# Performance work log

Hardware: AMD Instinct MI355X
Metric: run time of the kernel (lower is better)

The kernel has to match this reference:

```python
import jax, jax.numpy as jnp
import numpy as np

B, T, E, H = 4, 2048, 1024, 16
DH = E // H  # head_size = 64


def setup_inputs() -> dict:
    key = jax.random.key(0)
    ks = jax.random.split(key, 6)
    s_in = 1.0 / np.sqrt(E)
    return {
        "x": jax.random.normal(ks[0], (B, T, E), dtype=jnp.float32),
        "Wq": jax.random.normal(ks[1], (H, E, DH), dtype=jnp.float32) * s_in,
        "Wk": jax.random.normal(ks[2], (H, E, DH), dtype=jnp.float32) * s_in,
        "Wv": jax.random.normal(ks[3], (H, E, DH), dtype=jnp.float32) * s_in,
        "Wp": jax.random.normal(ks[4], (E, E), dtype=jnp.float32) * s_in,
        "bp": jax.random.normal(ks[5], (E,), dtype=jnp.float32) * 0.01,
    }


def reference(x, Wq, Wk, Wv, Wp, bp):
    # per-head q/k/v projections, batched over heads: [B,H,T,DH]
    q = jnp.einsum("bte,hed->bhtd", x, Wq)
    k = jnp.einsum("bte,hed->bhtd", x, Wk)
    v = jnp.einsum("bte,hed->bhtd", x, Wv)
    scale = 1.0 / jnp.sqrt(jnp.asarray(DH, dtype=x.dtype))
    scores = jnp.einsum("bhsd,bhtd->bhst", q, k) * scale  # [B,H,T,T]
    causal = jnp.tril(jnp.ones((T, T), dtype=bool))
    scores = jnp.where(causal, scores, jnp.asarray(-jnp.inf, dtype=scores.dtype))
    att = jax.nn.softmax(scores, axis=-1)
    out = jnp.einsum("bhst,bhtd->bhsd", att, v)  # [B,H,T,DH]
    # concat heads along last dim -> [B,T,E]
    out = out.transpose(0, 2, 1, 3).reshape(B, T, E)
    # output projection (dropout p=0.0 is identity)
    return out @ Wp.T + bp
```

## Files before the change

### kernel.cpp

```cpp
#include <hip/hip_runtime.h>
#include <hip/hip_bf16.h>

#define B_ 4
#define T_ 2048
#define E_ 1024
#define H_ 16
#define DH_ 64

typedef __bf16 bf16x8 __attribute__((ext_vector_type(8)));
typedef __bf16 bf16x4 __attribute__((ext_vector_type(4)));
typedef float f32x4 __attribute__((ext_vector_type(4)));

#define EXP2F(x) __builtin_amdgcn_exp2f(x)
#define NEG_INF (-__builtin_inff())

__device__ __forceinline__ void async_copy16(const __bf16* g, __bf16* l) {
    __builtin_amdgcn_global_load_lds(
        (const __attribute__((address_space(1))) unsigned int*)g,
        (__attribute__((address_space(3))) unsigned int*)l, 16, 0, 0);
}

__global__ void cast_f32_to_bf16(const float* __restrict__ src,
                                 __bf16* __restrict__ dst, int n) {
    int i = (blockIdx.x * blockDim.x + threadIdx.x) * 4;
    if (i + 3 < n) {
        float4 f = *reinterpret_cast<const float4*>(src + i);
        bf16x4 o = { (__bf16)f.x, (__bf16)f.y, (__bf16)f.z, (__bf16)f.w };
        *reinterpret_cast<bf16x4*>(dst + i) = o;
    }
}

__global__ void cast_wcat(const float* __restrict__ Wq, const float* __restrict__ Wk,
                          const float* __restrict__ Wv, __bf16* __restrict__ out) {
    int idx = blockIdx.x * blockDim.x + threadIdx.x;
    int e = idx & (E_ - 1);
    int n = idx >> 10;
    int rem = n & 1023, h = rem >> 6, d = rem & 63;
    const float* src = (n < 1024) ? Wq : (n < 2048 ? Wk : Wv);
    out[idx] = (__bf16)src[((h << 10) + e) * DH_ + d];
}

template<int MODE>
__global__ __launch_bounds__(256, 3) void gemm128(
    const __bf16* __restrict__ A, const __bf16* __restrict__ Bt,
    float* __restrict__ Cf, const float* __restrict__ bias,
    __bf16* __restrict__ oq, __bf16* __restrict__ ok, __bf16* __restrict__ ovt,
    int K, int N) {

    __shared__ __bf16 As[128][64];
    __shared__ __bf16 Bs[128][64];

    int tid = threadIdx.x, lane = tid & 63, wid = tid >> 6;
    int wr = wid >> 1, wc = wid & 1;
    int rlo = lane & 15, rhi = lane >> 4;
    int l8 = lane >> 3, c = lane & 7;

    const __bf16* Ab = A + (long)blockIdx.x * 128 * K;
    const __bf16* Bb = Bt + (long)blockIdx.y * 128 * K;

    f32x4 acc[4][4] = {};

    for (int k0 = 0; k0 < K; k0 += 64) {
        #pragma unroll
        for (int p = 0; p < 4; p++) {
            int gr = p * 32 + wid * 8 + l8;
            int sc = c ^ (gr & 7);
            async_copy16(Ab + (long)gr * K + k0 + sc * 8, &As[p * 32 + wid * 8][0]);
        }
        #pragma unroll
        for (int p = 0; p < 4; p++) {
            int gr = p * 32 + wid * 8 + l8;
            int sc = c ^ (gr & 7);
            async_copy16(Bb + (long)gr * K + k0 + sc * 8, &Bs[p * 32 + wid * 8][0]);
        }
        __syncthreads();

        #pragma unroll
        for (int kk = 0; kk < 2; kk++) {
            bf16x8 af[4], bfr[4];
            #pragma unroll
            for (int mi = 0; mi < 4; mi++) {
                int r = wr * 64 + mi * 16 + rlo;
                af[mi] = *reinterpret_cast<const bf16x8*>(
                    &As[r][((kk * 4 + rhi) ^ (r & 7)) * 8]);
            }
            #pragma unroll
            for (int ni = 0; ni < 4; ni++) {
                int r = wc * 64 + ni * 16 + rlo;
                bfr[ni] = *reinterpret_cast<const bf16x8*>(
                    &Bs[r][((kk * 4 + rhi) ^ (r & 7)) * 8]);
            }
            #pragma unroll
            for (int mi = 0; mi < 4; mi++)
                #pragma unroll
                for (int ni = 0; ni < 4; ni++)
                    acc[mi][ni] = __builtin_amdgcn_mfma_f32_16x16x32_bf16(
                        af[mi], bfr[ni], acc[mi][ni], 0, 0, 0);
        }
        __syncthreads();
    }

    long m0 = (long)blockIdx.x * 128 + wr * 64;
    int n0 = blockIdx.y * 128 + wc * 64;

    if constexpr (MODE == 1) {
        #pragma unroll
        for (int mi = 0; mi < 4; mi++) {
            #pragma unroll
            for (int ni = 0; ni < 4; ni++) {
                int cn = n0 + ni * 16 + rlo;
                #pragma unroll
                for (int r = 0; r < 4; r++) {
                    long rm = m0 + mi * 16 + rhi * 4 + r;
                    Cf[rm * N + cn] = acc[mi][ni][r] + bias[cn];
                }
            }
        }
    } else {
        int type = blockIdx.y >> 3;
        #pragma unroll
        for (int mi = 0; mi < 4; mi++) {
            long m_ = m0 + mi * 16 + rhi * 4;
            int b = (int)(m_ >> 11);
            int t0 = (int)(m_ & 2047);
            #pragma unroll
            for (int ni = 0; ni < 4; ni++) {
                int n = n0 + ni * 16 + rlo;
                int rem = n & 1023, h = rem >> 6, d = rem & 63;
                long bh = b * 16 + h;
                if (type == 2) {
                    bf16x4 o = { (__bf16)acc[mi][ni][0], (__bf16)acc[mi][ni][1],
                                 (__bf16)acc[mi][ni][2], (__bf16)acc[mi][ni][3] };
                    *reinterpret_cast<bf16x4*>(ovt + (bh * 64 + d) * 2048 + t0) = o;
                } else {
                    __bf16* dst = (type ? ok : oq) + bh * 2048 * 64;
                    #pragma unroll
                    for (int r = 0; r < 4; r++)
                        dst[(long)(t0 + r) * 64 + d] = (__bf16)acc[mi][ni][r];
                }
            }
        }
    }
}

__global__ __launch_bounds__(256, 4) void attn_kernel(
    const __bf16* __restrict__ q, const __bf16* __restrict__ k,
    const __bf16* __restrict__ vt, __bf16* __restrict__ attout) {

    __shared__ __bf16 Ks[2][64][64];
    __shared__ __bf16 Vs[2][64][64];
    __shared__ __bf16 Pl[4][16][64];

    int tid = threadIdx.x, lane = tid & 63, wid = tid >> 6;
    int rlo = lane & 15, rhi = lane >> 4;

    int fid = blockIdx.y * 16 + blockIdx.x;
    int xcd = fid & 7, slot = fid >> 3;
    int bh = xcd * 8 + (slot >> 4);
    int p = slot & 15;
    int tA = 31 - p, tB = p;

    int b = bh >> 4, h = bh & 15;
    const __bf16* qb = q + (long)bh * T_ * DH_;
    const __bf16* kb = k + (long)bh * T_ * DH_;
    const __bf16* vtb = vt + (long)bh * T_ * DH_;

    const float SCL = 0.125f * 1.44269504088896340736f;

    int srow = wid * 16 + (lane >> 3);
    int sc0 = (lane & 7) ^ (srow & 7);

    bf16x8 aqA[2], aqB[2];
    {
        long qrA = (long)tA * 64 + wid * 16 + rlo;
        aqA[0] = *reinterpret_cast<const bf16x8*>(qb + qrA * DH_ + 8 * rhi);
        aqA[1] = *reinterpret_cast<const bf16x8*>(qb + qrA * DH_ + 32 + 8 * rhi);
        long qrB = (long)tB * 64 + wid * 16 + rlo;
        aqB[0] = *reinterpret_cast<const bf16x8*>(qb + qrB * DH_ + 8 * rhi);
        aqB[1] = *reinterpret_cast<const bf16x8*>(qb + qrB * DH_ + 32 + 8 * rhi);
    }

    float mA = NEG_INF, lAc = 0.f, mB = NEG_INF, lBc = 0.f;
    f32x4 oA[4] = {}, oB[4] = {};

    auto STAGE = [&](int bs, int t) {
        const __bf16* ksrc = kb + (long)(t * 64 + srow) * DH_ + sc0 * 8;
        async_copy16(ksrc,           &Ks[bs][wid * 16][0]);
        async_copy16(ksrc + 8 * DH_, &Ks[bs][wid * 16 + 8][0]);
        const __bf16* vsrc = vtb + (long)srow * T_ + t * 64 + sc0 * 8;
        async_copy16(vsrc,           &Vs[bs][wid * 16][0]);
        async_copy16(vsrc + 8 * T_,  &Vs[bs][wid * 16 + 8][0]);
    };

    auto APPLYMASK = [&](f32x4* s, int qrow, int kt0) {
        int kbase = kt0 + rhi * 4;
        #pragma unroll
        for (int f = 0; f < 4; f++)
            #pragma unroll
            for (int r = 0; r < 4; r++)
                if (kbase + f * 16 + r > qrow) s[f][r] = NEG_INF;
    };

    auto SOFTMAX_PV = [&](int bs, f32x4* s, float& m_, float& l_, f32x4* o) {
        float pm;
        {
            f32x4 mx;
            #pragma unroll
            for (int r = 0; r < 4; r++)
                mx[r] = fmaxf(fmaxf(s[0][r], s[1][r]), fmaxf(s[2][r], s[3][r]));
            pm = fmaxf(fmaxf(mx[0], mx[1]), fmaxf(mx[2], mx[3]));
            pm = fmaxf(pm, __shfl_xor(pm, 16));
            pm = fmaxf(pm, __shfl_xor(pm, 32));
        }
        float pms = pm * SCL;

        bool need = !__all(pms <= m_ + 8.f);
        if (need) {
            float nm = fmaxf(m_, pms);
            float so = EXP2F(m_ - nm);
            m_ = nm;
            l_ *= so;
            float sov[4];
            #pragma unroll
            for (int r = 0; r < 4; r++) sov[r] = __shfl(so, rhi * 4 + r);
            #pragma unroll
            for (int fd = 0; fd < 4; fd++)
                #pragma unroll
                for (int r = 0; r < 4; r++)
                    o[fd][r] *= sov[r];
        }

        float rsum = 0.f;
        #pragma unroll
        for (int f = 0; f < 4; f++)
            #pragma unroll
            for (int r = 0; r < 4; r++) {
                float pv = EXP2F(fmaf(s[f][r], SCL, -m_));
                s[f][r] = pv;
                rsum += pv;
            }
        rsum += __shfl_xor(rsum, 16);
        rsum += __shfl_xor(rsum, 32);
        l_ += rsum;

        #pragma unroll
        for (int f = 0; f < 4; f++) {
            bf16x4 pw = { (__bf16)s[f][0], (__bf16)s[f][1],
                          (__bf16)s[f][2], (__bf16)s[f][3] };
            int keyb = f * 16 + rhi * 4;
            int c16 = keyb >> 3, sub = (keyb >> 2) & 1;
            *reinterpret_cast<bf16x4*>(
                &Pl[wid][rlo][((c16 ^ (rlo & 7)) << 3) + (sub << 2)]) = pw;
        }

        __builtin_amdgcn_s_setprio(1);
        #pragma unroll
        for (int kk = 0; kk < 2; kk++) {
            int ck = kk * 4 + rhi;
            bf16x8 ap = *reinterpret_cast<const bf16x8*>(&Pl[wid][rlo][(ck ^ (rlo & 7)) * 8]);
            #pragma unroll
            for (int fd = 0; fd < 4; fd++) {
                int vr = fd * 16 + rlo;
                bf16x8 bv = *reinterpret_cast<const bf16x8*>(
                    &Vs[bs][vr][(ck ^ (vr & 7)) * 8]);
                o[fd] = __builtin_amdgcn_mfma_f32_16x16x32_bf16(ap, bv, o[fd], 0, 0, 0);
            }
        }
        __builtin_amdgcn_s_setprio(0);
    };

    int qrowA = tA * 64 + wid * 16 + rlo;
    int qrowB = tB * 64 + wid * 16 + rlo;

    int nsteps = tA + 1;

    STAGE(0, 0);
    STAGE(1, 1);
    asm volatile("s_waitcnt vmcnt(4)" ::: "memory");
    asm volatile("s_barrier" ::: "memory");

    for (int t = 0; t < nsteps; ++t) {
        int cur = t & 1;
        bool doB = (t <= tB);

        f32x4 sA[4], sB[4];
        __builtin_amdgcn_s_setprio(1);
        #pragma unroll
        for (int f = 0; f < 4; f++) {
            int kr = f * 16 + rlo;
            bf16x8 ak0 = *reinterpret_cast<const bf16x8*>(
                &Ks[cur][kr][((0 + rhi) ^ (kr & 7)) * 8]);
            bf16x8 ak1 = *reinterpret_cast<const bf16x8*>(
                &Ks[cur][kr][((4 + rhi) ^ (kr & 7)) * 8]);
            f32x4 a0 = {};
            a0 = __builtin_amdgcn_mfma_f32_16x16x32_bf16(ak0, aqA[0], a0, 0, 0, 0);
            a0 = __builtin_amdgcn_mfma_f32_16x16x32_bf16(ak1, aqA[1], a0, 0, 0, 0);
            sA[f] = a0;
            if (doB) {
                f32x4 b0 = {};
                b0 = __builtin_amdgcn_mfma_f32_16x16x32_bf16(ak0, aqB[0], b0, 0, 0, 0);
                b0 = __builtin_amdgcn_mfma_f32_16x16x32_bf16(ak1, aqB[1], b0, 0, 0, 0);
                sB[f] = b0;
            }
        }
        __builtin_amdgcn_s_setprio(0);

        if (t == tA) APPLYMASK(sA, qrowA, t * 64);
        SOFTMAX_PV(cur, sA, mA, lAc, oA);
        if (doB) {
            if (t == tB) APPLYMASK(sB, qrowB, t * 64);
            SOFTMAX_PV(cur, sB, mB, lBc, oB);
        }

        asm volatile("s_barrier" ::: "memory");
        if (t + 2 < nsteps) {
            STAGE(cur, t + 2);
            asm volatile("s_waitcnt vmcnt(4)" ::: "memory");
        } else {
            asm volatile("s_waitcnt vmcnt(0)" ::: "memory");
        }
        asm volatile("s_barrier" ::: "memory");
    }

    float lvA[4], lvB[4];
    #pragma unroll
    for (int r = 0; r < 4; r++) {
        lvA[r] = __shfl(lAc, rhi * 4 + r);
        lvB[r] = __shfl(lBc, rhi * 4 + r);
    }
    #pragma unroll
    for (int r = 0; r < 4; r++) {
        float invA = 1.f / lvA[r];
        float invB = 1.f / lvB[r];
        long qrA = (long)tA * 64 + wid * 16 + rhi * 4 + r;
        long qrB = (long)tB * 64 + wid * 16 + rhi * 4 + r;
        #pragma unroll
        for (int fd = 0; fd < 4; fd++) {
            int d = fd * 16 + rlo;
            attout[((long)b * T_ + qrA) * E_ + h * DH_ + d] = (__bf16)(oA[fd][r] * invA);
            attout[((long)b * T_ + qrB) * E_ + h * DH_ + d] = (__bf16)(oB[fd][r] * invB);
        }
    }
}

extern "C" void kernel_launch(void* const* d_in, const int* in_sizes, int n_in,
                              void* d_out, int out_size, void* d_ws, size_t ws_size,
                              hipStream_t stream) {
    const float* x  = (const float*)d_in[0];
    const float* Wq = (const float*)d_in[1];
    const float* Wk = (const float*)d_in[2];
    const float* Wv = (const float*)d_in[3];
    const float* Wp = (const float*)d_in[4];
    const float* bp = (const float*)d_in[5];

    char* ws = (char*)d_ws;
    const long SZ_XE = (long)B_ * T_ * E_ * 2;
    __bf16* xb   = (__bf16*)(ws);
    __bf16* qb   = (__bf16*)(ws + SZ_XE);
    __bf16* kb   = (__bf16*)(ws + 2 * SZ_XE);
    __bf16* vt   = (__bf16*)(ws + 3 * SZ_XE);
    __bf16* wcat = (__bf16*)(ws + 4 * SZ_XE);
    __bf16* wpb  = (__bf16*)(ws + 4 * SZ_XE + (long)3072 * 1024 * 2);
    __bf16* att  = xb;

    cast_f32_to_bf16<<<8192, 256, 0, stream>>>(x, xb, B_ * T_ * E_);
    cast_wcat<<<12288, 256, 0, stream>>>(Wq, Wk, Wv, wcat);
    cast_f32_to_bf16<<<1024, 256, 0, stream>>>(Wp, wpb, E_ * E_);

    gemm128<3><<<dim3(64, 24), 256, 0, stream>>>(
        xb, wcat, nullptr, nullptr, qb, kb, vt, E_, 3 * E_);

    attn_kernel<<<dim3(16, B_ * H_), 256, 0, stream>>>(qb, kb, vt, att);

    gemm128<1><<<dim3(64, 8), 256, 0, stream>>>(
        att, wpb, (float*)d_out, bp, nullptr, nullptr, nullptr, E_, E_);
}
```

Measured before the change: 164.7 us.

## Fuse three cast kernels into one and defer softmax cross-lane reductions

Merges the x, Wq/Wk/Wv, and Wp casts into a single kernel launch, with the weight transpose-cast now handling 4 elements per thread. In the attention softmax, the row-max shuffle reduction runs only when a rescale is needed, and the row-sum shuffles move out of the loop to a single reduction at the end. This removes two launches and per-tile shuffle work, at the cost of strided scalar loads in the weight cast and per-lane max thresholds that rely on the lazy-rescale tolerance.

```diff
diff --git a/kernel.cpp b/kernel.cpp
--- a/kernel.cpp
+++ b/kernel.cpp
@@ -20,24 +20,34 @@
         (__attribute__((address_space(3))) unsigned int*)l, 16, 0, 0);
 }
 
-__global__ void cast_f32_to_bf16(const float* __restrict__ src,
-                                 __bf16* __restrict__ dst, int n) {
-    int i = (blockIdx.x * blockDim.x + threadIdx.x) * 4;
-    if (i + 3 < n) {
-        float4 f = *reinterpret_cast<const float4*>(src + i);
+__global__ void cast_all(const float* __restrict__ x,
+                         const float* __restrict__ Wq, const float* __restrict__ Wk,
+                         const float* __restrict__ Wv, const float* __restrict__ Wp,
+                         __bf16* __restrict__ xb, __bf16* __restrict__ wcat,
+                         __bf16* __restrict__ wpb) {
+    int tid = blockIdx.x * blockDim.x + threadIdx.x;
+    {
+        int i = tid * 4;
+        float4 f = *reinterpret_cast<const float4*>(x + i);
         bf16x4 o = { (__bf16)f.x, (__bf16)f.y, (__bf16)f.z, (__bf16)f.w };
-        *reinterpret_cast<bf16x4*>(dst + i) = o;
-    }
-}
-
-__global__ void cast_wcat(const float* __restrict__ Wq, const float* __restrict__ Wk,
-                          const float* __restrict__ Wv, __bf16* __restrict__ out) {
-    int idx = blockIdx.x * blockDim.x + threadIdx.x;
-    int e = idx & (E_ - 1);
-    int n = idx >> 10;
-    int rem = n & 1023, h = rem >> 6, d = rem & 63;
-    const float* src = (n < 1024) ? Wq : (n < 2048 ? Wk : Wv);
-    out[idx] = (__bf16)src[((h << 10) + e) * DH_ + d];
+        *reinterpret_cast<bf16x4*>(xb + i) = o;
+    }
+    if (tid < 262144) {
+        int i = tid * 4;
+        float4 f = *reinterpret_cast<const float4*>(Wp + i);
+        bf16x4 o = { (__bf16)f.x, (__bf16)f.y, (__bf16)f.z, (__bf16)f.w };
+        *reinterpret_cast<bf16x4*>(wpb + i) = o;
+    }
+    if (tid < 786432) {
+        int i = tid * 4;
+        int e = i & (E_ - 1);
+        int n = i >> 10;
+        int rem = n & 1023, h = rem >> 6, d = rem & 63;
+        const float* src = (n < 1024) ? Wq : (n < 2048 ? Wk : Wv);
+        const float* sp = src + ((long)((h << 10) + e)) * DH_ + d;
+        bf16x4 o = { (__bf16)sp[0], (__bf16)sp[DH_], (__bf16)sp[2 * DH_], (__bf16)sp[3 * DH_] };
+        *reinterpret_cast<bf16x4*>(wcat + i) = o;
+    }
 }
 
 template<int MODE>
@@ -202,21 +212,18 @@
     };
 
     auto SOFTMAX_PV = [&](int bs, f32x4* s, float& m_, float& l_, f32x4* o) {
-        float pm;
-        {
-            f32x4 mx;
-            #pragma unroll
-            for (int r = 0; r < 4; r++)
-                mx[r] = fmaxf(fmaxf(s[0][r], s[1][r]), fmaxf(s[2][r], s[3][r]));
-            pm = fmaxf(fmaxf(mx[0], mx[1]), fmaxf(mx[2], mx[3]));
-            pm = fmaxf(pm, __shfl_xor(pm, 16));
-            pm = fmaxf(pm, __shfl_xor(pm, 32));
-        }
-        float pms = pm * SCL;
+        f32x4 mx;
+        #pragma unroll
+        for (int r = 0; r < 4; r++)
+            mx[r] = fmaxf(fmaxf(s[0][r], s[1][r]), fmaxf(s[2][r], s[3][r]));
+        float pml = fmaxf(fmaxf(mx[0], mx[1]), fmaxf(mx[2], mx[3]));
+        float pms = pml * SCL;
 
         bool need = !__all(pms <= m_ + 8.f);
         if (need) {
-            float nm = fmaxf(m_, pms);
+            float pr = fmaxf(pms, __shfl_xor(pms, 16));
+            pr = fmaxf(pr, __shfl_xor(pr, 32));
+            float nm = fmaxf(m_, pr);
             float so = EXP2F(m_ - nm);
             m_ = nm;
             l_ *= so;
@@ -239,8 +246,6 @@
                 s[f][r] = pv;
                 rsum += pv;
             }
-        rsum += __shfl_xor(rsum, 16);
-        rsum += __shfl_xor(rsum, 32);
         l_ += rsum;
 
         #pragma unroll
@@ -322,6 +327,11 @@
         asm volatile("s_barrier" ::: "memory");
     }
 
+    lAc += __shfl_xor(lAc, 16);
+    lAc += __shfl_xor(lAc, 32);
+    lBc += __shfl_xor(lBc, 16);
+    lBc += __shfl_xor(lBc, 32);
+
     float lvA[4], lvB[4];
     #pragma unroll
     for (int r = 0; r < 4; r++) {
@@ -363,9 +373,7 @@
     __bf16* wpb  = (__bf16*)(ws + 4 * SZ_XE + (long)3072 * 1024 * 2);
     __bf16* att  = xb;
 
-    cast_f32_to_bf16<<<8192, 256, 0, stream>>>(x, xb, B_ * T_ * E_);
-    cast_wcat<<<12288, 256, 0, stream>>>(Wq, Wk, Wv, wcat);
-    cast_f32_to_bf16<<<1024, 256, 0, stream>>>(Wp, wpb, E_ * E_);
+    cast_all<<<8192, 256, 0, stream>>>(x, Wq, Wk, Wv, Wp, xb, wcat, wpb);
 
     gemm128<3><<<dim3(64, 24), 256, 0, stream>>>(
         xb, wcat, nullptr, nullptr, qb, kb, vt, E_, 3 * E_);
```

Result: faster. 158.8 us, median of 2 (-3.6%).
